# Kernel tuning notes

Measured on AMD Instinct MI355X. Metric: run time of the kernel, lower is better.

## Reference

```python
import jax, jax.numpy as jnp
import numpy as np

EPS = 1e-5

def _conv(x, w, b, pad):
    # x: [B,C,H,W], w: [O,I,kh,kw] -> [B,O,H',W']
    y = jax.lax.conv_general_dilated(x, w, (1, 1), pad,
                                     dimension_numbers=('NCHW', 'OIHW', 'NCHW'))
    return y + b[None, :, None, None]

def _bn(x, g, b, m, v):
    # inference-mode BatchNorm2d
    s = g / jnp.sqrt(v + EPS)
    return x * s[None, :, None, None] + (b - m * s)[None, :, None, None]

def setup_inputs():
    key = jax.random.key(0)
    ks = jax.random.split(key, 8)
    N, Cin, Cout, H, W, BS = 2, 64, 256, 512, 512, 32
    GH, GW = H // BS, W // BS
    nB = 256
    x = jax.random.normal(ks[0], (N, Cin, H, W), jnp.float32)
    rng = np.random.default_rng(0)
    flat = rng.choice(N * GH * GW, size=nB, replace=False)  # unique blocks
    idx = np.stack([flat // (GH * GW), (flat // GW) % GH, flat % GW], axis=1).astype(np.int32)
    indices = jnp.asarray(idx)             # [nB, 3] = (batch, block_row, block_col)
    mask = jnp.zeros((N, GH, GW), jnp.bool_).at[indices[:, 0], indices[:, 1], indices[:, 2]].set(True)
    def wgt(k, shape):
        return jax.random.normal(k, shape, jnp.float32) * 0.05
    z, o = jnp.zeros(Cout, jnp.float32), jnp.ones(Cout, jnp.float32)
    params = dict(
        w1=wgt(ks[1], (Cout, Cin, 1, 1)), b1=z, g1=o, be1=z, m1=z, v1=o,
        w2=wgt(ks[2], (Cout, Cout, 3, 3)), b2=z, g2=o, be2=z, m2=z, v2=o,
        w3=wgt(ks[3], (Cout, Cout, 1, 1)), b3=z, g3=o, be3=z, m3=z, v3=o,
        wd=wgt(ks[4], (Cout, Cin, 1, 1)), bd=z,
    )
    return {"x": x, "mask": mask, "indices": indices, **params,
            "block_size": 32, "block_stride": 32, "block_offset": 0}

def reference(x, mask, indices, w1, b1, g1, be1, m1, v1,
              w2, b2, g2, be2, m2, v2, w3, b3, g3, be3, m3, v3,
              wd, bd, block_size, block_stride, block_offset):
    BS = block_size
    N, Cin, H, W = x.shape
    b = indices[:, 0]
    rows = indices[:, 1, None] * block_stride + block_offset + jnp.arange(BS)  # [nB,BS]
    cols = indices[:, 2, None] * block_stride + block_offset + jnp.arange(BS)  # [nB,BS]
    ci = jnp.arange(Cin)
    # SparseGather: [nB, Cin, BS, BS]
    blocks = x[b[:, None, None, None], ci[None, :, None, None],
               rows[:, None, :, None], cols[:, None, None, :]]
    h = jax.nn.relu(_bn(_conv(blocks, w1, b1, 'VALID'), g1, be1, m1, v1))
    dense_y = jax.nn.relu(_bn(_conv(h, w2, b2, 'SAME'), g2, be2, m2, v2))
    # conv3/bn3 in the original are dead code (inplace-relu aliasing): output unused.
    ybase = _conv(x, wd, bd, 'VALID')  # downsample (in_channels != out_channels)
    Cout = ybase.shape[1]
    co = jnp.arange(Cout)
    # SparseScatter (add=False -> overwrite blocks; indices are unique)
    y = ybase.at[b[:, None, None, None], co[None, :, None, None],
                 rows[:, None, :, None], cols[:, None, None, :]].set(dense_y)
    return y
```

## Files before the change

kernel.cpp:

```cpp
#include <hip/hip_runtime.h>

#define HW 262144
#define EPSF 1e-5f

typedef __attribute__((ext_vector_type(8))) short bf16x8;
typedef __attribute__((ext_vector_type(4))) float f32x4;

__device__ __forceinline__ unsigned short f2bf(float f) {
    unsigned u = __builtin_bit_cast(unsigned, f);
    return (unsigned short)((u + 0x7FFFu + ((u >> 16) & 1u)) >> 16);
}

typedef __attribute__((address_space(3))) unsigned lds_u32_t;
typedef __attribute__((address_space(1))) const unsigned glb_u32_t;
__device__ __forceinline__ void dma16(const void* gsrc, void* ldst) {
    __builtin_amdgcn_global_load_lds((glb_u32_t*)gsrc, (lds_u32_t*)ldst, 16, 0, 0);
}

#define W2WS_OFF 0
#define W1WS_OFF 1212416
#define T1WS_OFF 1249280
#define S2WS_OFF 1250304
#define T2WS_OFF 1251328
#define WDWS_OFF 1252352
#define MSKWS_OFF 1289216

__global__ __launch_bounds__(512) void kmask(const int* __restrict__ indices,
                                             int nB, char* __restrict__ ws) {
    unsigned char* mb = (unsigned char*)(ws + MSKWS_OFF);
    const int t = threadIdx.x;
    if (t < 512) mb[t] = 0;
    __syncthreads();
    if (t < nB) {
        int bn = indices[t*3+0], gh = indices[t*3+1], gw = indices[t*3+2];
        if ((unsigned)bn < 2u && (unsigned)gh < 16u && (unsigned)gw < 16u)
            mb[bn*256 + gh*16 + gw] = 1;
    }
}

__global__ __launch_bounds__(256) void kprep(
    const float* __restrict__ w1, const float* __restrict__ b1,
    const float* __restrict__ g1, const float* __restrict__ be1,
    const float* __restrict__ m1, const float* __restrict__ v1,
    const float* __restrict__ w2, const float* __restrict__ b2,
    const float* __restrict__ g2, const float* __restrict__ be2,
    const float* __restrict__ m2, const float* __restrict__ v2,
    const float* __restrict__ wd,
    char* __restrict__ ws)
{
    unsigned short* w2ws = (unsigned short*)(ws + W2WS_OFF);
    unsigned short* w1ws = (unsigned short*)(ws + W1WS_OFF);
    unsigned short* wdws = (unsigned short*)(ws + WDWS_OFF);
    float* t1ws = (float*)(ws + T1WS_OFF);
    float* s2ws = (float*)(ws + S2WS_OFF);
    float* t2ws = (float*)(ws + T2WS_OFF);

    const int bid = blockIdx.x, t = threadIdx.x;
    if (bid < 2304) {
        int e  = bid*256 + t;
        int hc = e & 31;
        int r1 = e >> 5;
        int tap = r1 % 9;
        int r2 = r1 / 9;
        int co = r2 & 63;
        int q  = r2 >> 6;
        int cz = q & 3, ch = q >> 2;
        float v = w2[(size_t)(cz*64+co)*2304 + (size_t)(ch*32+hc)*9 + tap];
        w2ws[((ch*4+cz)*64+co)*296 + tap*32 + hc] = f2bf(v);
    } else if (bid < 2368) {
        int e = (bid-2304)*256 + t;
        int hc = e >> 6, ci = e & 63;
        float s1 = g1[hc] * rsqrtf(v1[hc] + EPSF);
        w1ws[hc*72 + ci] = f2bf(w1[hc*64+ci] * s1);
    } else if (bid < 2432) {
        int e = (bid-2368)*256 + t;
        int co = e >> 6, ci = e & 63;
        wdws[co*72 + ci] = f2bf(wd[co*64 + ci]);
    } else {
        if (t < 256) {
            float s1 = g1[t] * rsqrtf(v1[t] + EPSF);
            t1ws[t] = (b1[t]-m1[t])*s1 + be1[t];
            float s2 = g2[t] * rsqrtf(v2[t] + EPSF);
            s2ws[t] = s2;
            t2ws[t] = (b2[t]-m2[t])*s2 + be2[t];
        }
    }
}

__global__ __launch_bounds__(256, 2) void k1_mfma(
    const float* __restrict__ x,
    const float* __restrict__ bd, const char* __restrict__ ws,
    const int* __restrict__ bstride, const int* __restrict__ boff,
    float* __restrict__ y)
{
    extern __shared__ char smem[];
    unsigned short* xT  = (unsigned short*)smem;
    unsigned short* wdS = (unsigned short*)(smem + 36864);
    float*          bdS = (float*)(smem + 73728);

    const int t = threadIdx.x, lane = t & 63, w = t >> 6;
    const int m = lane & 15, g = lane >> 4;
    const int bid = blockIdx.x;
    const int n   = bid >> 10;
    const int row = (bid >> 1) & 511;
    const int c0  = (bid & 1) * 256;

    #pragma unroll
    for (int i = 0; i < 9; ++i)
        dma16((const char*)ws + WDWS_OFF + (t + i*256)*16,
              (char*)wdS + (t + i*256)*16);
    if (t < 64) dma16((const char*)bd + t*16, (char*)bdS + t*16);

    const size_t xbase = (size_t)n*64*HW + (size_t)row*512 + c0;
    #pragma unroll 4
    for (int jc = 0; jc < 16; ++jc) {
        int ci = w + 4*jc;
        float4 xv = *(const float4*)&x[xbase + (size_t)ci*HW + lane*4];
        xT[(lane*4+0)*72 + ci] = f2bf(xv.x);
        xT[(lane*4+1)*72 + ci] = f2bf(xv.y);
        xT[(lane*4+2)*72 + ci] = f2bf(xv.z);
        xT[(lane*4+3)*72 + ci] = f2bf(xv.w);
    }

    const int stride = bstride[0], off = boff[0];
    const bool safe = (stride == 32) && (off == 0);
    unsigned long long mv = 0;
    if (safe) {
        const unsigned char* mb = (const unsigned char*)(ws + MSKWS_OFF);
        mv = *(const unsigned long long*)&mb[n*256 + (row>>5)*16 + (bid&1)*8];
    }

    __syncthreads();

    bf16x8 bF[2][4];
    #pragma unroll
    for (int pxf = 0; pxf < 4; ++pxf)
        #pragma unroll
        for (int kk = 0; kk < 2; ++kk)
            bF[kk][pxf] = *(const bf16x8*)&xT[(w*64 + pxf*16 + m)*72 + kk*32 + g*8];

    const size_t ybase = (size_t)(n*256)*HW + (size_t)row*512 + c0;
    #pragma unroll 1
    for (int cof = 0; cof < 16; ++cof) {
        bf16x8 a0 = *(const bf16x8*)&wdS[(cof*16+m)*72 +      g*8];
        bf16x8 a1 = *(const bf16x8*)&wdS[(cof*16+m)*72 + 32 + g*8];
        f32x4 ac[4];
        #pragma unroll
        for (int pxf = 0; pxf < 4; ++pxf) {
            ac[pxf] = (f32x4){0.f,0.f,0.f,0.f};
            ac[pxf] = __builtin_amdgcn_mfma_f32_16x16x32_bf16(a0, bF[0][pxf], ac[pxf], 0, 0, 0);
            ac[pxf] = __builtin_amdgcn_mfma_f32_16x16x32_bf16(a1, bF[1][pxf], ac[pxf], 0, 0, 0);
        }
        #pragma unroll
        for (int pxf = 0; pxf < 4; ++pxf) {
            const int pxg = w*4 + pxf;
            const bool skip = safe && (((mv >> ((pxg>>1)*8)) & 0xffull) != 0ull);
            if (!skip) {
                #pragma unroll
                for (int j = 0; j < 4; ++j) {
                    const int co = cof*16 + g*4 + j;
                    y[ybase + (size_t)co*HW + pxg*16 + m] = ac[pxf][j] + bdS[co];
                }
            }
        }
    }
}

#define DMA_W2(CH, CZ, BUF)                                                   \
    {                                                                         \
        const char* ws2_ = (const char*)w2ws + (size_t)((CH)*4 + (CZ))*37888; \
        _Pragma("unroll")                                                     \
        for (int i2_ = 0; i2_ < 4; ++i2_)                                     \
            dma16(ws2_ + t*16 + i2_*8192, (char*)(BUF) + t*16 + i2_*8192);    \
        if (t < 320) dma16(ws2_ + t*16 + 32768, (char*)(BUF) + t*16 + 32768); \
    }

#define CONV2_CZ(CZ, BUF)                                                     \
    {                                                                         \
        __builtin_amdgcn_s_setprio(1);                                        \
        _Pragma("unroll")                                                     \
        for (int tap = 0; tap < 9; ++tap) {                                   \
            const int dy = tap/3, dx = tap%3;                                 \
            bf16x8 aF[4];                                                     \
            _Pragma("unroll")                                                 \
            for (int cof = 0; cof < 4; ++cof)                                 \
                aF[cof] = *(const bf16x8*)&(BUF)[(cof*16 + m)*296 + tap*32 + g*8]; \
            _Pragma("unroll")                                                 \
            for (int pxf = 0; pxf < 2; ++pxf) {                               \
                int p_ = (w + dy)*34 + pxf*16 + m + dx;                       \
                bf16x8 bFr = *(const bf16x8*)&hS[p_*40 + g*8];                \
                _Pragma("unroll")                                             \
                for (int cof = 0; cof < 4; ++cof)                             \
                    acc[CZ][pxf][cof] = __builtin_amdgcn_mfma_f32_16x16x32_bf16( \
                        aF[cof], bFr, acc[CZ][pxf][cof], 0, 0, 0);            \
            }                                                                 \
        }                                                                     \
        __builtin_amdgcn_s_setprio(0);                                        \
    }

__global__ __launch_bounds__(512, 2) void k2_fused(
    const float* __restrict__ x, const int* __restrict__ indices,
    const char* __restrict__ ws,
    const int* __restrict__ bstride, const int* __restrict__ boff,
    float* __restrict__ y)
{
    extern __shared__ char smem[];
    unsigned short* xT  = (unsigned short*)smem;
    unsigned short* w1s = (unsigned short*)(smem + 50688);
    unsigned short* hS  = (unsigned short*)(smem + 55296);
    unsigned short* w2A = (unsigned short*)(smem + 83456);
    unsigned short* w2B = (unsigned short*)(smem + 121344);
    float* t1S = (float*)(smem + 159232);
    float* s2S = (float*)(smem + 160256);
    float* t2S = (float*)(smem + 161280);

    const unsigned short* w2ws = (const unsigned short*)(ws + W2WS_OFF);
    const unsigned short* w1ws = (const unsigned short*)(ws + W1WS_OFF);

    const int t    = threadIdx.x;
    const int lane = t & 63;
    const int w    = t >> 6;
    const int m    = lane & 15;
    const int g    = lane >> 4;

    const int bid = blockIdx.x;
    const int blk = bid >> 2, pz = bid & 3;
    const int bn = indices[blk*3+0], gr = indices[blk*3+1], gc = indices[blk*3+2];
    const int stride = bstride[0], off = boff[0];
    const int row0 = gr*stride + off, col0 = gc*stride + off;

    if (t < 192) {
        const float* src = (t < 64) ? (const float*)(ws + T1WS_OFF)
                         : (t < 128) ? (const float*)(ws + S2WS_OFF)
                                     : (const float*)(ws + T2WS_OFF);
        float* dst = (t < 64) ? t1S : (t < 128) ? s2S : t2S;
        dma16(src + (lane)*4, dst + (lane)*4);
    }

    {
        const int half = lane >> 5, cc = lane & 31;
        for (int pb = w*80; pb < w*80 + 80; pb += 2) {
            int pi = pb + half;
            int r = pi >> 6, ci = pi & 63;
            int br = pz*8 + r - 1;
            if ((unsigned)br < 32u) {
                float xv = x[(size_t)bn*64*HW + (size_t)ci*HW
                             + (size_t)(row0+br)*512 + (col0+cc)];
                xT[(r*34 + cc + 1)*72 + ci] = f2bf(xv);
            }
        }
    }

    f32x4 acc[4][2][4];
    #pragma unroll
    for (int a = 0; a < 4; ++a)
        #pragma unroll
        for (int b = 0; b < 2; ++b)
            #pragma unroll
            for (int c = 0; c < 4; ++c) acc[a][b][c] = (f32x4){0.f,0.f,0.f,0.f};

    #pragma unroll 1
    for (int ch = 0; ch < 8; ++ch) {
        __syncthreads();

        if (t < 288) dma16((const char*)w1ws + ch*4608 + t*16, (char*)w1s + t*16);
        DMA_W2(ch, 0, w2A);
        DMA_W2(ch, 1, w2B);
        __syncthreads();

        f32x4 a1[3][2];
        #pragma unroll
        for (int i = 0; i < 3; ++i) { a1[i][0] = (f32x4){0,0,0,0}; a1[i][1] = (f32x4){0,0,0,0}; }
        #pragma unroll
        for (int i = 0; i < 3; ++i) {
            const int tile = w*3 + i;
            if (tile < 22) {
                #pragma unroll
                for (int kk = 0; kk < 2; ++kk) {
                    bf16x8 bF = *(const bf16x8*)&xT[(tile*16 + m)*72 + kk*32 + g*8];
                    #pragma unroll
                    for (int hct = 0; hct < 2; ++hct) {
                        bf16x8 aF = *(const bf16x8*)&w1s[(hct*16 + m)*72 + kk*32 + g*8];
                        a1[i][hct] = __builtin_amdgcn_mfma_f32_16x16x32_bf16(
                                         aF, bF, a1[i][hct], 0, 0, 0);
                    }
                }
            }
        }
        #pragma unroll
        for (int i = 0; i < 3; ++i) {
            const int tile = w*3 + i;
            if (tile < 22) {
                int p = tile*16 + m;
                int r = p / 34;
                int c = p - r*34;
                int br = pz*8 + r - 1;
                bool valid = (c >= 1) && (c <= 32) && ((unsigned)br < 32u);
                #pragma unroll
                for (int hct = 0; hct < 2; ++hct) {
                    unsigned short hv[4];
                    #pragma unroll
                    for (int j = 0; j < 4; ++j) {
                        float tv = t1S[ch*32 + hct*16 + g*4 + j];
                        float hf = fmaxf(a1[i][hct][j] + tv, 0.f);
                        hv[j] = valid ? f2bf(hf) : (unsigned short)0;
                    }
                    unsigned lo = (unsigned)hv[0] | ((unsigned)hv[1] << 16);
                    unsigned hi = (unsigned)hv[2] | ((unsigned)hv[3] << 16);
                    *(uint2*)&hS[p*40 + hct*16 + g*4] = make_uint2(lo, hi);
                }
            }
        }
        __syncthreads();

        CONV2_CZ(0, w2A);
        __syncthreads();
        DMA_W2(ch, 2, w2A);
        CONV2_CZ(1, w2B);
        __syncthreads();
        DMA_W2(ch, 3, w2B);
        CONV2_CZ(2, w2A);
        __syncthreads();
        CONV2_CZ(3, w2B);
    }

    const size_t ybase = (size_t)bn*256*HW + (size_t)(row0 + pz*8 + w)*512 + col0;
    #pragma unroll
    for (int cz = 0; cz < 4; ++cz) {
        #pragma unroll
        for (int cof = 0; cof < 4; ++cof) {
            #pragma unroll
            for (int j = 0; j < 4; ++j) {
                const int co = cz*64 + cof*16 + g*4 + j;
                float s2 = s2S[co], t2 = t2S[co];
                #pragma unroll
                for (int pxf = 0; pxf < 2; ++pxf) {
                    y[ybase + (size_t)co*HW + pxf*16 + m] =
                        fmaxf(fmaf(acc[cz][pxf][cof][j], s2, t2), 0.f);
                }
            }
        }
    }
}

extern "C" void kernel_launch(void* const* d_in, const int* in_sizes, int n_in,
                              void* d_out, int out_size, void* d_ws, size_t ws_size,
                              hipStream_t stream) {
    const float* x       = (const float*)d_in[0];
    const int*   indices = (const int*)  d_in[2];
    const float* w1  = (const float*)d_in[3];
    const float* b1  = (const float*)d_in[4];
    const float* g1  = (const float*)d_in[5];
    const float* be1 = (const float*)d_in[6];
    const float* m1  = (const float*)d_in[7];
    const float* v1  = (const float*)d_in[8];
    const float* w2  = (const float*)d_in[9];
    const float* b2  = (const float*)d_in[10];
    const float* g2  = (const float*)d_in[11];
    const float* be2 = (const float*)d_in[12];
    const float* m2  = (const float*)d_in[13];
    const float* v2  = (const float*)d_in[14];
    const float* wd  = (const float*)d_in[21];
    const float* bd  = (const float*)d_in[22];
    const int* bstride = (const int*)d_in[24];
    const int* boff    = (const int*)d_in[25];
    float* y = (float*)d_out;
    char* ws = (char*)d_ws;

    const int nB = in_sizes[2] / 3;

    hipLaunchKernelGGL(kmask, dim3(1), dim3(512), 0, stream, indices, nB, ws);
    hipLaunchKernelGGL(kprep, dim3(2433), dim3(256), 0, stream,
                       w1, b1, g1, be1, m1, v1, w2, b2, g2, be2, m2, v2, wd, ws);
    hipLaunchKernelGGL(k1_mfma, dim3(2048), dim3(256), 74752, stream,
                       x, bd, ws, bstride, boff, y);
    hipLaunchKernelGGL(k2_fused, dim3(nB * 4), dim3(512), 162304, stream,
                       x, indices, ws, bstride, boff, y);
}
```

Baseline: 504.1 us.

## Split conv2 warps into output-channel groups with 2-row pixel tiles, single weight buffer

Conv2 work is re-partitioned so each warp covers a 64-channel output group and 2 rows × 32 pixels instead of all 256 channels for one row. Each weight fragment is now reused across four pixel fragments instead of two. The two 37 KB double buffers become one 75 KB buffer loaded twice per channel chunk. This drops the overlap between weight DMA and MFMA work and serializes load then compute with extra barriers, in exchange for better register reuse and fewer sync rounds.

After: 462.7 us. 1.09x faster.

```diff
diff --git a/kernel.cpp b/kernel.cpp
--- a/kernel.cpp
+++ b/kernel.cpp
@@ -166,16 +166,17 @@
     }
 }
 
-#define DMA_W2(CH, CZ, BUF)                                                   \
+#define DMA_CZH(CH, CZH)                                                      \
     {                                                                         \
-        const char* ws2_ = (const char*)w2ws + (size_t)((CH)*4 + (CZ))*37888; \
+        const char* s_ = (const char*)w2ws                                    \
+                         + (size_t)(CH)*151552 + (size_t)(CZH)*75776;         \
         _Pragma("unroll")                                                     \
-        for (int i2_ = 0; i2_ < 4; ++i2_)                                     \
-            dma16(ws2_ + t*16 + i2_*8192, (char*)(BUF) + t*16 + i2_*8192);    \
-        if (t < 320) dma16(ws2_ + t*16 + 32768, (char*)(BUF) + t*16 + 32768); \
-    }
-
-#define CONV2_CZ(CZ, BUF)                                                     \
+        for (int i_ = 0; i_ < 9; ++i_)                                        \
+            dma16(s_ + t*16 + i_*8192, (char*)w2S + t*16 + i_*8192);          \
+        if (t < 128) dma16(s_ + 73728 + t*16, (char*)w2S + 73728 + t*16);     \
+    }
+
+#define CONV2_CZH(CZH)                                                        \
     {                                                                         \
         __builtin_amdgcn_s_setprio(1);                                        \
         _Pragma("unroll")                                                     \
@@ -184,15 +185,16 @@
             bf16x8 aF[4];                                                     \
             _Pragma("unroll")                                                 \
             for (int cof = 0; cof < 4; ++cof)                                 \
-                aF[cof] = *(const bf16x8*)&(BUF)[(cof*16 + m)*296 + tap*32 + g*8]; \
+                aF[cof] = *(const bf16x8*)&w2S[(cog*64 + cof*16 + m)*296      \
+                                               + tap*32 + g*8];               \
             _Pragma("unroll")                                                 \
-            for (int pxf = 0; pxf < 2; ++pxf) {                               \
-                int p_ = (w + dy)*34 + pxf*16 + m + dx;                       \
+            for (int pxf = 0; pxf < 4; ++pxf) {                               \
+                int p_ = (ph*2 + (pxf>>1) + dy)*34 + (pxf&1)*16 + m + dx;     \
                 bf16x8 bFr = *(const bf16x8*)&hS[p_*40 + g*8];                \
                 _Pragma("unroll")                                             \
                 for (int cof = 0; cof < 4; ++cof)                             \
-                    acc[CZ][pxf][cof] = __builtin_amdgcn_mfma_f32_16x16x32_bf16( \
-                        aF[cof], bFr, acc[CZ][pxf][cof], 0, 0, 0);            \
+                    acc[CZH][cof][pxf] = __builtin_amdgcn_mfma_f32_16x16x32_bf16( \
+                        aF[cof], bFr, acc[CZH][cof][pxf], 0, 0, 0);           \
             }                                                                 \
         }                                                                     \
         __builtin_amdgcn_s_setprio(0);                                        \
@@ -208,8 +210,7 @@
     unsigned short* xT  = (unsigned short*)smem;
     unsigned short* w1s = (unsigned short*)(smem + 50688);
     unsigned short* hS  = (unsigned short*)(smem + 55296);
-    unsigned short* w2A = (unsigned short*)(smem + 83456);
-    unsigned short* w2B = (unsigned short*)(smem + 121344);
+    unsigned short* w2S = (unsigned short*)(smem + 83456);
     float* t1S = (float*)(smem + 159232);
     float* s2S = (float*)(smem + 160256);
     float* t2S = (float*)(smem + 161280);
@@ -222,6 +223,8 @@
     const int w    = t >> 6;
     const int m    = lane & 15;
     const int g    = lane >> 4;
+    const int cog  = w >> 2;
+    const int ph   = w & 3;
 
     const int bid = blockIdx.x;
     const int blk = bid >> 2, pz = bid & 3;
@@ -251,11 +254,11 @@
         }
     }
 
-    f32x4 acc[4][2][4];
+    f32x4 acc[2][4][4];
     #pragma unroll
-    for (int a = 0; a < 4; ++a)
-        #pragma unroll
-        for (int b = 0; b < 2; ++b)
+    for (int a = 0; a < 2; ++a)
+        #pragma unroll
+        for (int b = 0; b < 4; ++b)
             #pragma unroll
             for (int c = 0; c < 4; ++c) acc[a][b][c] = (f32x4){0.f,0.f,0.f,0.f};
 
@@ -264,8 +267,7 @@
         __syncthreads();
 
         if (t < 288) dma16((const char*)w1ws + ch*4608 + t*16, (char*)w1s + t*16);
-        DMA_W2(ch, 0, w2A);
-        DMA_W2(ch, 1, w2B);
+        DMA_CZH(ch, 0);
         __syncthreads();
 
         f32x4 a1[3][2];
@@ -313,30 +315,29 @@
         }
         __syncthreads();
 
-        CONV2_CZ(0, w2A);
-        __syncthreads();
-        DMA_W2(ch, 2, w2A);
-        CONV2_CZ(1, w2B);
-        __syncthreads();
-        DMA_W2(ch, 3, w2B);
-        CONV2_CZ(2, w2A);
-        __syncthreads();
-        CONV2_CZ(3, w2B);
-    }
-
-    const size_t ybase = (size_t)bn*256*HW + (size_t)(row0 + pz*8 + w)*512 + col0;
+        CONV2_CZH(0);
+        __syncthreads();
+        DMA_CZH(ch, 1);
+        __syncthreads();
+        CONV2_CZH(1);
+    }
+
+    const size_t yblk = (size_t)bn*256*HW;
+    const int rbase = row0 + pz*8 + ph*2;
     #pragma unroll
-    for (int cz = 0; cz < 4; ++cz) {
+    for (int czh = 0; czh < 2; ++czh) {
         #pragma unroll
         for (int cof = 0; cof < 4; ++cof) {
             #pragma unroll
             for (int j = 0; j < 4; ++j) {
-                const int co = cz*64 + cof*16 + g*4 + j;
+                const int co = czh*128 + cog*64 + cof*16 + g*4 + j;
                 float s2 = s2S[co], t2 = t2S[co];
                 #pragma unroll
-                for (int pxf = 0; pxf < 2; ++pxf) {
-                    y[ybase + (size_t)co*HW + pxf*16 + m] =
-                        fmaxf(fmaf(acc[cz][pxf][cof][j], s2, t2), 0.f);
+                for (int pxf = 0; pxf < 4; ++pxf) {
+                    const int rr = rbase + (pxf>>1);
+                    const int cc2 = col0 + (pxf&1)*16 + m;
+                    y[yblk + (size_t)co*HW + (size_t)rr*512 + cc2] =
+                        fmaxf(fmaf(acc[czh][cof][pxf][j], s2, t2), 0.f);
                 }
             }
         }
```
